# Kernel optimization log

Measured on AMD Instinct MI355X. Metric: run time of the kernel, lower is better.

The kernel has to match this reference:

```python
import jax, jax.numpy as jnp
import numpy as np

B, QN, KVN = 4, 512, 512
QD, KD, H, VD = 512, 512, 256, 256


def setup_inputs() -> dict:
    key = jax.random.key(0)
    ks = jax.random.split(key, 6)
    q = jax.random.normal(ks[0], (B, QN, QD), dtype=jnp.float32)
    k = jax.random.normal(ks[1], (B, KVN, KD), dtype=jnp.float32)
    v = jax.random.normal(ks[2], (B, KVN, VD), dtype=jnp.float32)
    # Linear weights (torch nn.Linear stores [out, in]; bias=False)
    Wq = jax.random.normal(ks[3], (H, QD), dtype=jnp.float32) / np.sqrt(QD)
    Wk = jax.random.normal(ks[4], (H, KD), dtype=jnp.float32) / np.sqrt(KD)
    wv = jax.random.normal(ks[5], (H,), dtype=jnp.float32) / np.sqrt(H)
    return {"q": q, "k": k, "v": v, "Wq": Wq, "Wk": Wk, "wv": wv}


def reference(q, k, v, Wq, Wk, wv):
    # Project queries and keys to hidden dim H
    qh = jnp.einsum("bqd,hd->bqh", q, Wq)  # [B, QN, H]
    kh = jnp.einsum("bkd,hd->bkh", k, Wk)  # [B, KVN, H]
    # Broadcast add + tanh: [B, QN, KVN, H]
    energy = jnp.tanh(qh[:, :, None, :] + kh[:, None, :, :])
    # Score projection to scalar per (q, kv) pair
    scores = jnp.einsum("bqkh,h->bqk", energy, wv)  # [B, QN, KVN]
    attention = jax.nn.softmax(scores, axis=-1)
    # Dropout omitted (inference mode)
    output = jnp.einsum("bqk,bkv->bqv", attention, v)  # [B, QN, VD]
    return (output, attention)
```

## Files before the change

kernel.cpp:

```cpp
#include <hip/hip_runtime.h>

#define B_ 4
#define QN 512
#define KVN 512
#define QD_ 512
#define H_ 256
#define VD_ 256

typedef __attribute__((ext_vector_type(8))) short bf16x8;
typedef __attribute__((ext_vector_type(4))) float f32x4;
typedef __attribute__((ext_vector_type(4))) unsigned short u16x4;
typedef unsigned short u16;

__device__ __forceinline__ float rcp_(float x) { return __builtin_amdgcn_rcpf(x); }
__device__ __forceinline__ float ex2_(float x) { return __builtin_amdgcn_exp2f(x); }

__device__ __forceinline__ u16 bf16_rne(float x) {
    unsigned u = __float_as_uint(x);
    unsigned r = u + 0x7FFFu + ((u >> 16) & 1u);
    return (u16)(r >> 16);
}
__device__ __forceinline__ void split2(float x, u16& h, u16& l) {
    h = bf16_rne(x);
    float hf = __uint_as_float((unsigned)h << 16);
    l = bf16_rne(x - hf);
}
__device__ __forceinline__ void split4(float4 a, u16x4& h, u16x4& l) {
    u16 hh, ll;
    split2(a.x, hh, ll); h[0] = hh; l[0] = ll;
    split2(a.y, hh, ll); h[1] = hh; l[1] = ll;
    split2(a.z, hh, ll); h[2] = hh; l[2] = ll;
    split2(a.w, hh, ll); h[3] = hh; l[3] = ll;
}

__global__ __launch_bounds__(256) void presplit(const float* __restrict__ q,
                                                const float* __restrict__ k,
                                                const float* __restrict__ Wq,
                                                const float* __restrict__ Wk,
                                                u16* __restrict__ q_hi, u16* __restrict__ q_lo,
                                                u16* __restrict__ k_hi, u16* __restrict__ k_lo,
                                                u16* __restrict__ w_hi, u16* __restrict__ w_lo) {
    const int NQ = 2048 * 512 / 4, NW = 256 * 512 / 4;
    int idx = blockIdx.x * 256 + threadIdx.x;
    const float* src; u16 *dh, *dl; int off;
    if (idx < NQ)             { src = q;  dh = q_hi; dl = q_lo; off = idx; }
    else if (idx < 2 * NQ)    { src = k;  dh = k_hi; dl = k_lo; off = idx - 2 * NQ + NQ; }
    else if (idx < 2 * NQ + NW) { src = Wq; dh = w_hi; dl = w_lo; off = idx - 2 * NQ; }
    else { src = Wk; dh = w_hi + 256 * 512; dl = w_lo + 256 * 512; off = idx - 2 * NQ - NW; }
    float4 v4 = ((const float4*)src)[off];
    u16x4 h, l;
    split4(v4, h, l);
    *(u16x4*)(dh + off * 4) = h;
    *(u16x4*)(dl + off * 4) = l;
}

__global__ __launch_bounds__(256) void vtrans(const float* __restrict__ v,
                                              u16* __restrict__ vt_hi,
                                              u16* __restrict__ vt_lo) {
    __shared__ float ts[64][65];
    const int b = blockIdx.z;
    const int j0 = blockIdx.x * 64, n0 = blockIdx.y * 64;
    const int tid = threadIdx.x;
#pragma unroll
    for (int t = 0; t < 4; ++t) {
        int idx = t * 256 + tid;
        int j = idx >> 4, nq = idx & 15;
        float4 v4 = *(const float4*)(v + ((size_t)b * KVN + j0 + j) * VD_ + n0 + nq * 4);
        *(float4*)&ts[j][nq * 4] = v4;
    }
    __syncthreads();
#pragma unroll
    for (int t = 0; t < 4; ++t) {
        int idx = t * 256 + tid;
        int jq = idx & 15, n = idx >> 4;
        u16x4 h, l;
        u16 hh, ll;
#pragma unroll
        for (int e = 0; e < 4; ++e) {
            split2(ts[jq * 4 + e][n], hh, ll);
            h[e] = hh; l[e] = ll;
        }
        size_t off = ((size_t)b * VD_ + n0 + n) * KVN + j0 + jq * 4;
        *(u16x4*)(vt_hi + off) = h;
        *(u16x4*)(vt_lo + off) = l;
    }
}

__global__ __launch_bounds__(256) void proj_mfma(const u16* __restrict__ q_hi, const u16* __restrict__ q_lo,
                                                 const u16* __restrict__ k_hi, const u16* __restrict__ k_lo,
                                                 const u16* __restrict__ w_hi, const u16* __restrict__ w_lo,
                                                 float* __restrict__ eq, float* __restrict__ ek) {
    const int z = blockIdx.z;
    const u16* __restrict__ Ah_g = z ? k_hi : q_hi;
    const u16* __restrict__ Al_g = z ? k_lo : q_lo;
    const u16* __restrict__ Bh_g = w_hi + (size_t)z * H_ * QD_;
    const u16* __restrict__ Bl_g = w_lo + (size_t)z * H_ * QD_;
    float* __restrict__ C = z ? ek : eq;
    __shared__ u16 Ash[4][32][8], Asl[4][32][8], Bsh[4][32][8], Bsl[4][32][8];
    const int tid = threadIdx.x;
    const int wave = tid >> 6, lane = tid & 63;
    const int fl = lane & 15, kg = lane >> 4;
    const int r0 = blockIdx.y * 32, c0 = blockIdx.x * 32;
    const int ar = 16 * (wave & 1), bc = 16 * (wave >> 1);
    const int frow = (tid & 127) >> 2, fkq = tid & 3, fsel = tid >> 7;
    f32x4 acc = {};
    for (int k0 = 0; k0 < QD_; k0 += 32) {
        __syncthreads();
        {
            const u16* as = (fsel ? Al_g : Ah_g) + (size_t)(r0 + frow) * QD_ + k0 + fkq * 8;
            u16* ad = fsel ? &Asl[fkq][frow][0] : &Ash[fkq][frow][0];
            *(uint4*)ad = *(const uint4*)as;
            const u16* bs = (fsel ? Bl_g : Bh_g) + (size_t)(c0 + frow) * QD_ + k0 + fkq * 8;
            u16* bd = fsel ? &Bsl[fkq][frow][0] : &Bsh[fkq][frow][0];
            *(uint4*)bd = *(const uint4*)bs;
        }
        __syncthreads();
        bf16x8 a_h = *(const bf16x8*)&Ash[kg][ar + fl][0];
        bf16x8 a_l = *(const bf16x8*)&Asl[kg][ar + fl][0];
        bf16x8 b_h = *(const bf16x8*)&Bsh[kg][bc + fl][0];
        bf16x8 b_l = *(const bf16x8*)&Bsl[kg][bc + fl][0];
        acc = __builtin_amdgcn_mfma_f32_16x16x32_bf16(a_h, b_h, acc, 0, 0, 0);
        acc = __builtin_amdgcn_mfma_f32_16x16x32_bf16(a_h, b_l, acc, 0, 0, 0);
        acc = __builtin_amdgcn_mfma_f32_16x16x32_bf16(a_l, b_h, acc, 0, 0, 0);
    }
    const float cs = 2.8853900817779268f;
    const int rg = kg * 4;
#pragma unroll
    for (int r = 0; r < 4; ++r)
        C[(size_t)(r0 + ar + rg + r) * H_ + c0 + bc + fl] = ex2_(acc[r] * cs);
}

__device__ __forceinline__ float grp4(float4 qv, float4 kv, float4 w4, float acc) {
    float a = __builtin_fmaf(qv.x, kv.x, 1.0f);
    float b = __builtin_fmaf(qv.y, kv.y, 1.0f);
    float c = __builtin_fmaf(qv.z, kv.z, 1.0f);
    float d = __builtin_fmaf(qv.w, kv.w, 1.0f);
    float ab = a * b, cd = c * d;
    float n1 = __builtin_fmaf(w4.y, a, w4.x * b);
    float n2 = __builtin_fmaf(w4.w, c, w4.z * d);
    float num = __builtin_fmaf(n2, ab, n1 * cd);
    return __builtin_fmaf(num, rcp_(ab * cd), acc);
}

__global__ __launch_bounds__(256, 4) void scores_kernel(const float* __restrict__ eq,
                                                        const float* __restrict__ ek,
                                                        const float* __restrict__ wv,
                                                        float* __restrict__ sc) {
    __shared__ float qs[16][68];
    __shared__ float ks[32][68];
    const int b = blockIdx.z;
    const int i0 = blockIdx.y * 16, j0 = blockIdx.x * 32;
    const int tid = threadIdx.x;
    const int wid = tid >> 6, lane = tid & 63;
    const int qr = (wid << 2) + (lane >> 4), kc = lane & 15;
    float acc0 = 0.f, acc1 = 0.f;
    for (int h0 = 0; h0 < H_; h0 += 64) {
        __syncthreads();
        {
            int r1 = tid >> 4, c1 = tid & 15;
            *(float4*)&qs[r1][c1 * 4] =
                *(const float4*)(eq + (size_t)(b * QN + i0 + r1) * H_ + h0 + c1 * 4);
#pragma unroll
            for (int t = 0; t < 2; ++t) {
                int idx = t * 256 + tid;
                int r2 = idx >> 4, c2 = idx & 15;
                *(float4*)&ks[r2][c2 * 4] =
                    *(const float4*)(ek + (size_t)(b * KVN + j0 + r2) * H_ + h0 + c2 * 4);
            }
        }
        __syncthreads();
#pragma unroll 4
        for (int hh = 0; hh < 64; hh += 4) {
            float4 w4 = *(const float4*)(wv + h0 + hh);
            float4 qv = *(const float4*)&qs[qr][hh];
            float4 k0v = *(const float4*)&ks[kc][hh];
            float4 k1v = *(const float4*)&ks[kc + 16][hh];
            acc0 = grp4(qv, k0v, w4, acc0);
            acc1 = grp4(qv, k1v, w4, acc1);
        }
    }
    sc[(size_t)(b * QN + i0 + qr) * KVN + j0 + kc] = -2.0f * acc0;
    sc[(size_t)(b * QN + i0 + qr) * KVN + j0 + kc + 16] = -2.0f * acc1;
}

__global__ __launch_bounds__(256) void softmax_kernel(float* __restrict__ attn,
                                                      u16* __restrict__ at_hi,
                                                      u16* __restrict__ at_lo) {
    int row = blockIdx.x;
    int tid = threadIdx.x;
    float* p = attn + (size_t)row * KVN;
    float x0 = p[tid], x1 = p[tid + 256];
    float m = fmaxf(x0, x1);
#pragma unroll
    for (int d = 1; d < 64; d <<= 1) m = fmaxf(m, __shfl_xor(m, d));
    __shared__ float redm[4], reds[4];
    int wave = tid >> 6, lane = tid & 63;
    if (lane == 0) redm[wave] = m;
    __syncthreads();
    m = fmaxf(fmaxf(redm[0], redm[1]), fmaxf(redm[2], redm[3]));
    float e0 = __expf(x0 - m), e1 = __expf(x1 - m);
    float s = e0 + e1;
#pragma unroll
    for (int d = 1; d < 64; d <<= 1) s += __shfl_xor(s, d);
    if (lane == 0) reds[wave] = s;
    __syncthreads();
    s = reds[0] + reds[1] + reds[2] + reds[3];
    float inv = rcp_(s);
    float r0v = e0 * inv, r1v = e1 * inv;
    p[tid] = r0v;
    p[tid + 256] = r1v;
    u16 h, l;
    size_t base = (size_t)row * KVN;
    split2(r0v, h, l);
    at_hi[base + tid] = h; at_lo[base + tid] = l;
    split2(r1v, h, l);
    at_hi[base + tid + 256] = h; at_lo[base + tid + 256] = l;
}

__global__ __launch_bounds__(256) void out_mfma(const u16* __restrict__ vt_hi, const u16* __restrict__ vt_lo,
                                                const u16* __restrict__ at_hi, const u16* __restrict__ at_lo,
                                                float* __restrict__ out) {
    const int b = blockIdx.z;
    const u16* __restrict__ Ah_g = vt_hi + (size_t)b * VD_ * KVN;
    const u16* __restrict__ Al_g = vt_lo + (size_t)b * VD_ * KVN;
    const u16* __restrict__ Bh_g = at_hi + (size_t)b * QN * KVN;
    const u16* __restrict__ Bl_g = at_lo + (size_t)b * QN * KVN;
    float* __restrict__ outb = out + (size_t)b * QN * VD_;
    __shared__ u16 Ash[4][32][8], Asl[4][32][8], Bsh[4][32][8], Bsl[4][32][8];
    const int tid = threadIdx.x;
    const int wave = tid >> 6, lane = tid & 63;
    const int fl = lane & 15, kg = lane >> 4;
    const int r0 = blockIdx.y * 32;
    const int c0 = blockIdx.x * 32;
    const int ar = 16 * (wave & 1), bc = 16 * (wave >> 1);
    const int frow = (tid & 127) >> 2, fkq = tid & 3, fsel = tid >> 7;
    f32x4 acc = {};
    for (int k0 = 0; k0 < KVN; k0 += 32) {
        __syncthreads();
        {
            const u16* as = (fsel ? Al_g : Ah_g) + (size_t)(r0 + frow) * KVN + k0 + fkq * 8;
            u16* ad = fsel ? &Asl[fkq][frow][0] : &Ash[fkq][frow][0];
            *(uint4*)ad = *(const uint4*)as;
            const u16* bs = (fsel ? Bl_g : Bh_g) + (size_t)(c0 + frow) * KVN + k0 + fkq * 8;
            u16* bd = fsel ? &Bsl[fkq][frow][0] : &Bsh[fkq][frow][0];
            *(uint4*)bd = *(const uint4*)bs;
        }
        __syncthreads();
        bf16x8 a_h = *(const bf16x8*)&Ash[kg][ar + fl][0];
        bf16x8 a_l = *(const bf16x8*)&Asl[kg][ar + fl][0];
        bf16x8 b_h = *(const bf16x8*)&Bsh[kg][bc + fl][0];
        bf16x8 b_l = *(const bf16x8*)&Bsl[kg][bc + fl][0];
        acc = __builtin_amdgcn_mfma_f32_16x16x32_bf16(a_h, b_h, acc, 0, 0, 0);
        acc = __builtin_amdgcn_mfma_f32_16x16x32_bf16(a_h, b_l, acc, 0, 0, 0);
        acc = __builtin_amdgcn_mfma_f32_16x16x32_bf16(a_l, b_h, acc, 0, 0, 0);
    }
    const int rg = kg * 4;
    float4 o = {acc[0], acc[1], acc[2], acc[3]};
    *(float4*)(outb + (size_t)(c0 + bc + fl) * VD_ + r0 + ar + rg) = o;
}

extern "C" void kernel_launch(void* const* d_in, const int* in_sizes, int n_in,
                              void* d_out, int out_size, void* d_ws, size_t ws_size,
                              hipStream_t stream) {
    const float* q  = (const float*)d_in[0];
    const float* k  = (const float*)d_in[1];
    const float* v  = (const float*)d_in[2];
    const float* Wq = (const float*)d_in[3];
    const float* Wk = (const float*)d_in[4];
    const float* wv = (const float*)d_in[5];
    float* out  = (float*)d_out;
    float* attn = out + (size_t)B_ * QN * VD_;

    float* eq = (float*)d_ws;
    float* ek = eq + 2048 * 256;
    u16* q_hi = (u16*)(ek + 2048 * 256);
    u16* q_lo = q_hi + 2048 * 512;
    u16* k_hi = q_lo + 2048 * 512;
    u16* k_lo = k_hi + 2048 * 512;
    u16* w_hi = k_lo + 2048 * 512;
    u16* w_lo = w_hi + 512 * 512;
    u16* vt_hi = w_lo + 512 * 512;
    u16* vt_lo = vt_hi + (size_t)B_ * VD_ * KVN;
    u16* at_hi = q_hi;
    u16* at_lo = q_lo;

    presplit<<<2304, 256, 0, stream>>>(q, k, Wq, Wk, q_hi, q_lo, k_hi, k_lo, w_hi, w_lo);
    vtrans<<<dim3(KVN / 64, VD_ / 64, B_), 256, 0, stream>>>(v, vt_hi, vt_lo);
    proj_mfma<<<dim3(H_ / 32, 2048 / 32, 2), 256, 0, stream>>>(q_hi, q_lo, k_hi, k_lo,
                                                               w_hi, w_lo, eq, ek);
    scores_kernel<<<dim3(KVN / 32, QN / 16, B_), 256, 0, stream>>>(eq, ek, wv, attn);
    softmax_kernel<<<B_ * QN, 256, 0, stream>>>(attn, at_hi, at_lo);
    out_mfma<<<dim3(QN / 32, VD_ / 32, B_), 256, 0, stream>>>(vt_hi, vt_lo, at_hi, at_lo, out);
}
```

Measured before the change: 73.83 us.

## Transpose query projection and use packed 2-wide math in scores kernel

The projection kernel now writes the exponentiated query projection transposed (H-major), so the scores kernel can read two adjacent query rows per thread straight from global memory instead of staging them in shared memory. Each thread now computes a 2x2 tile (two query rows by two key rows) using 2-wide float vector FMAs that can map to packed FP32 instructions. The block tile grows to 32x32. This increases per-thread reuse and is meant to cut LDS traffic and instruction count in the tanh-sum inner loop. The cost is uncached global reads of the query values in the inner loop and scalar reciprocals that remain unpacked.

```diff
diff --git a/kernel.cpp b/kernel.cpp
--- a/kernel.cpp
+++ b/kernel.cpp
@@ -6,9 +6,11 @@
 #define QD_ 512
 #define H_ 256
 #define VD_ 256
+#define TOTR 2048
 
 typedef __attribute__((ext_vector_type(8))) short bf16x8;
 typedef __attribute__((ext_vector_type(4))) float f32x4;
+typedef __attribute__((ext_vector_type(2))) float f32x2;
 typedef __attribute__((ext_vector_type(4))) unsigned short u16x4;
 typedef unsigned short u16;
 
@@ -89,13 +91,12 @@
 __global__ __launch_bounds__(256) void proj_mfma(const u16* __restrict__ q_hi, const u16* __restrict__ q_lo,
                                                  const u16* __restrict__ k_hi, const u16* __restrict__ k_lo,
                                                  const u16* __restrict__ w_hi, const u16* __restrict__ w_lo,
-                                                 float* __restrict__ eq, float* __restrict__ ek) {
+                                                 float* __restrict__ eqT, float* __restrict__ ek) {
     const int z = blockIdx.z;
     const u16* __restrict__ Ah_g = z ? k_hi : q_hi;
     const u16* __restrict__ Al_g = z ? k_lo : q_lo;
     const u16* __restrict__ Bh_g = w_hi + (size_t)z * H_ * QD_;
     const u16* __restrict__ Bl_g = w_lo + (size_t)z * H_ * QD_;
-    float* __restrict__ C = z ? ek : eq;
     __shared__ u16 Ash[4][32][8], Asl[4][32][8], Bsh[4][32][8], Bsl[4][32][8];
     const int tid = threadIdx.x;
     const int wave = tid >> 6, lane = tid & 63;
@@ -125,62 +126,69 @@
     }
     const float cs = 2.8853900817779268f;
     const int rg = kg * 4;
-#pragma unroll
-    for (int r = 0; r < 4; ++r)
-        C[(size_t)(r0 + ar + rg + r) * H_ + c0 + bc + fl] = ex2_(acc[r] * cs);
-}
-
-__device__ __forceinline__ float grp4(float4 qv, float4 kv, float4 w4, float acc) {
-    float a = __builtin_fmaf(qv.x, kv.x, 1.0f);
-    float b = __builtin_fmaf(qv.y, kv.y, 1.0f);
-    float c = __builtin_fmaf(qv.z, kv.z, 1.0f);
-    float d = __builtin_fmaf(qv.w, kv.w, 1.0f);
-    float ab = a * b, cd = c * d;
-    float n1 = __builtin_fmaf(w4.y, a, w4.x * b);
-    float n2 = __builtin_fmaf(w4.w, c, w4.z * d);
-    float num = __builtin_fmaf(n2, ab, n1 * cd);
-    return __builtin_fmaf(num, rcp_(ab * cd), acc);
-}
-
-__global__ __launch_bounds__(256, 4) void scores_kernel(const float* __restrict__ eq,
+    if (z == 0) {
+        float4 o = {ex2_(acc[0] * cs), ex2_(acc[1] * cs), ex2_(acc[2] * cs), ex2_(acc[3] * cs)};
+        *(float4*)(eqT + (size_t)(c0 + bc + fl) * TOTR + r0 + ar + rg) = o;
+    } else {
+#pragma unroll
+        for (int r = 0; r < 4; ++r)
+            ek[(size_t)(r0 + ar + rg + r) * H_ + c0 + bc + fl] = ex2_(acc[r] * cs);
+    }
+}
+
+__device__ __forceinline__ f32x2 col4(const f32x2* qp, float4 kc, float4 w4, f32x2 acc) {
+    const f32x2 one = {1.0f, 1.0f};
+    f32x2 d0 = __builtin_elementwise_fma(qp[0], (f32x2){kc.x, kc.x}, one);
+    f32x2 d1 = __builtin_elementwise_fma(qp[1], (f32x2){kc.y, kc.y}, one);
+    f32x2 d2 = __builtin_elementwise_fma(qp[2], (f32x2){kc.z, kc.z}, one);
+    f32x2 d3 = __builtin_elementwise_fma(qp[3], (f32x2){kc.w, kc.w}, one);
+    f32x2 ab = d0 * d1, cd = d2 * d3;
+    f32x2 n1 = __builtin_elementwise_fma((f32x2){w4.y, w4.y}, d0, (f32x2){w4.x, w4.x} * d1);
+    f32x2 n2 = __builtin_elementwise_fma((f32x2){w4.w, w4.w}, d2, (f32x2){w4.z, w4.z} * d3);
+    f32x2 num = __builtin_elementwise_fma(n2, ab, n1 * cd);
+    f32x2 den = ab * cd;
+    f32x2 r = {rcp_(den.x), rcp_(den.y)};
+    return __builtin_elementwise_fma(num, r, acc);
+}
+
+__global__ __launch_bounds__(256, 4) void scores_kernel(const float* __restrict__ eqT,
                                                         const float* __restrict__ ek,
                                                         const float* __restrict__ wv,
                                                         float* __restrict__ sc) {
-    __shared__ float qs[16][68];
     __shared__ float ks[32][68];
     const int b = blockIdx.z;
-    const int i0 = blockIdx.y * 16, j0 = blockIdx.x * 32;
+    const int i0 = blockIdx.y * 32, j0 = blockIdx.x * 32;
     const int tid = threadIdx.x;
-    const int wid = tid >> 6, lane = tid & 63;
-    const int qr = (wid << 2) + (lane >> 4), kc = lane & 15;
-    float acc0 = 0.f, acc1 = 0.f;
+    const int qg = tid & 15, kg = tid >> 4;
+    const int row0 = b * QN + i0 + 2 * qg;
+    f32x2 acc0 = {0.f, 0.f}, acc1 = {0.f, 0.f};
     for (int h0 = 0; h0 < H_; h0 += 64) {
         __syncthreads();
-        {
-            int r1 = tid >> 4, c1 = tid & 15;
-            *(float4*)&qs[r1][c1 * 4] =
-                *(const float4*)(eq + (size_t)(b * QN + i0 + r1) * H_ + h0 + c1 * 4);
-#pragma unroll
-            for (int t = 0; t < 2; ++t) {
-                int idx = t * 256 + tid;
-                int r2 = idx >> 4, c2 = idx & 15;
-                *(float4*)&ks[r2][c2 * 4] =
-                    *(const float4*)(ek + (size_t)(b * KVN + j0 + r2) * H_ + h0 + c2 * 4);
-            }
-        }
-        __syncthreads();
-#pragma unroll 4
+#pragma unroll
+        for (int t = 0; t < 2; ++t) {
+            int idx = t * 256 + tid;
+            int row = idx >> 4, c4 = idx & 15;
+            *(float4*)&ks[row][c4 * 4] =
+                *(const float4*)(ek + (size_t)(b * KVN + j0 + row) * H_ + h0 + c4 * 4);
+        }
+        __syncthreads();
+#pragma unroll 8
         for (int hh = 0; hh < 64; hh += 4) {
             float4 w4 = *(const float4*)(wv + h0 + hh);
-            float4 qv = *(const float4*)&qs[qr][hh];
-            float4 k0v = *(const float4*)&ks[kc][hh];
-            float4 k1v = *(const float4*)&ks[kc + 16][hh];
-            acc0 = grp4(qv, k0v, w4, acc0);
-            acc1 = grp4(qv, k1v, w4, acc1);
-        }
-    }
-    sc[(size_t)(b * QN + i0 + qr) * KVN + j0 + kc] = -2.0f * acc0;
-    sc[(size_t)(b * QN + i0 + qr) * KVN + j0 + kc + 16] = -2.0f * acc1;
+            f32x2 qp[4];
+#pragma unroll
+            for (int e = 0; e < 4; ++e)
+                qp[e] = *(const f32x2*)(eqT + (size_t)(h0 + hh + e) * TOTR + row0);
+            float4 kc0 = *(const float4*)&ks[2 * kg][hh];
+            float4 kc1 = *(const float4*)&ks[2 * kg + 1][hh];
+            acc0 = col4(qp, kc0, w4, acc0);
+            acc1 = col4(qp, kc1, w4, acc1);
+        }
+    }
+    f32x2 s0 = {-2.0f * acc0.x, -2.0f * acc1.x};
+    f32x2 s1 = {-2.0f * acc0.y, -2.0f * acc1.y};
+    *(f32x2*)(sc + (size_t)row0 * KVN + j0 + 2 * kg) = s0;
+    *(f32x2*)(sc + (size_t)(row0 + 1) * KVN + j0 + 2 * kg) = s1;
 }
 
 __global__ __launch_bounds__(256) void softmax_kernel(float* __restrict__ attn,
@@ -271,9 +279,9 @@
     float* out  = (float*)d_out;
     float* attn = out + (size_t)B_ * QN * VD_;
 
-    float* eq = (float*)d_ws;
-    float* ek = eq + 2048 * 256;
-    u16* q_hi = (u16*)(ek + 2048 * 256);
+    float* eqT = (float*)d_ws;
+    float* ek  = eqT + H_ * TOTR;
+    u16* q_hi = (u16*)(ek + TOTR * H_);
     u16* q_lo = q_hi + 2048 * 512;
     u16* k_hi = q_lo + 2048 * 512;
     u16* k_lo = k_hi + 2048 * 512;
@@ -287,8 +295,8 @@
     presplit<<<2304, 256, 0, stream>>>(q, k, Wq, Wk, q_hi, q_lo, k_hi, k_lo, w_hi, w_lo);
     vtrans<<<dim3(KVN / 64, VD_ / 64, B_), 256, 0, stream>>>(v, vt_hi, vt_lo);
     proj_mfma<<<dim3(H_ / 32, 2048 / 32, 2), 256, 0, stream>>>(q_hi, q_lo, k_hi, k_lo,
-                                                               w_hi, w_lo, eq, ek);
-    scores_kernel<<<dim3(KVN / 32, QN / 16, B_), 256, 0, stream>>>(eq, ek, wv, attn);
+                                                               w_hi, w_lo, eqT, ek);
+    scores_kernel<<<dim3(KVN / 32, QN / 32, B_), 256, 0, stream>>>(eqT, ek, wv, attn);
     softmax_kernel<<<B_ * QN, 256, 0, stream>>>(attn, at_hi, at_lo);
     out_mfma<<<dim3(QN / 32, VD_ / 32, B_), 256, 0, stream>>>(vt_hi, vt_lo, at_hi, at_lo, out);
 }
```

Result: slower. 93.04 us (+26.0%).
